# Kernel optimization log

Measured on AMD Instinct MI355X. Metric: run time of the kernel, lower is better.

The kernel has to match this reference:

```python
import jax, jax.numpy as jnp
import numpy as np

EPS = 1e-5  # PyTorch BatchNorm2d default eps


def _batchnorm(x, gamma, beta):
    # training-mode BN over (N, T, V) per channel; x: [N, C, T, V]
    mean = jnp.mean(x, axis=(0, 2, 3), keepdims=True)
    var = jnp.var(x, axis=(0, 2, 3), keepdims=True)
    inv = jax.lax.rsqrt(var + EPS)
    return (x - mean) * inv * gamma[None, :, None, None] + beta[None, :, None, None]


def setup_inputs() -> dict:
    key = jax.random.key(0)
    ks = jax.random.split(key, 8)
    N, Cin, Cout, T, V, S = 64, 64, 128, 300, 25, 3
    x = jax.random.normal(ks[0], (N, Cin, T, V), dtype=jnp.float32)
    A = jax.random.uniform(ks[1], (S, V, V), dtype=jnp.float32)
    # per-subset 1x1 conv weights/biases (kaiming-ish scale)
    W = jax.random.normal(ks[2], (S, Cout, Cin), dtype=jnp.float32) / np.sqrt(Cin)
    b = jax.random.normal(ks[3], (S, Cout), dtype=jnp.float32) * 0.01
    alpha = jnp.zeros((1,), dtype=jnp.float32)
    bn_gamma = jnp.ones((Cout,), dtype=jnp.float32)
    bn_beta = jnp.zeros((Cout,), dtype=jnp.float32)
    # residual down path (in_channels != out_channels): conv1x1 + BN
    down_W = jax.random.normal(ks[4], (Cout, Cin), dtype=jnp.float32) / np.sqrt(Cin)
    down_b = jax.random.normal(ks[5], (Cout,), dtype=jnp.float32) * 0.01
    down_gamma = jnp.ones((Cout,), dtype=jnp.float32)
    down_beta = jnp.zeros((Cout,), dtype=jnp.float32)
    return {
        "x": x, "A": A, "W": W, "b": b, "alpha": alpha,
        "bn_gamma": bn_gamma, "bn_beta": bn_beta,
        "down_W": down_W, "down_b": down_b,
        "down_gamma": down_gamma, "down_beta": down_beta,
    }


def reference(x, A, W, b, alpha, bn_gamma, bn_beta, down_W, down_b, down_gamma, down_beta):
    V = x.shape[-1]
    eye = jnp.eye(V, dtype=x.dtype)
    A_adj = A + alpha[0] * eye[None]  # [S, V, V]
    # sum_s conv1x1_s( x @ A_s ): fuse adjacency matmul, 1x1 conv, subset sum
    y_agg = jnp.einsum('nctv,svw,soc->notw', x, A_adj, W)
    y_agg = y_agg + jnp.sum(b, axis=0)[None, :, None, None]
    y = _batchnorm(y_agg, bn_gamma, bn_beta)
    # residual down: 1x1 conv + BN (in_channels != out_channels)
    res = jnp.einsum('nctv,oc->notv', x, down_W) + down_b[None, :, None, None]
    res = _batchnorm(res, down_gamma, down_beta)
    return jax.nn.relu(y + res)
```

## Files before the change

kernel.cpp:

```cpp
#include <hip/hip_runtime.h>
#include <hip/hip_bf16.h>

#define N_   64
#define CIN  64
#define COUT 128
#define T_   300
#define V_   25
#define S_   3
#define NTV  (N_ * T_ * V_)

#define TS     10
#define NTB    (T_ / TS)
#define NBLK   (N_ * NTB)
#define RED_ROWS   64
#define RED_BLOCKS (NBLK / RED_ROWS)

#define WS_P    0
#define WS_P2   (WS_P + NBLK * 512)
#define WS_COEF (WS_P2 + RED_BLOCKS * 512)
#define WS_WF   (WS_COEF + 512)
#define WS_WSF  (WS_WF + 16384)
#define WS_AF   (WS_WSF + 16384)

typedef __attribute__((ext_vector_type(8))) short short8;
typedef __attribute__((ext_vector_type(4))) float f32x4;

__device__ __forceinline__ unsigned short bfbits(float f) {
    union { __hip_bfloat16 h; unsigned short u; } cv;
    cv.h = __float2bfloat16(f);
    return cv.u;
}
__device__ __forceinline__ unsigned int pack2(float lo, float hi) {
    return (unsigned int)bfbits(lo) | ((unsigned int)bfbits(hi) << 16);
}

__device__ __forceinline__ int zoff(int nl, int k) {
    int slot = (k >> 3) ^ (nl & 31);
    return nl * 512 + slot * 16 + (k & 7) * 2;
}

__global__ __launch_bounds__(256) void k_prep(const float* __restrict__ W,
                                              const float* __restrict__ dW,
                                              const float* __restrict__ A,
                                              const float* __restrict__ alpha,
                                              unsigned short* __restrict__ Wf,
                                              unsigned short* __restrict__ Af) {
    int i = blockIdx.x * 256 + threadIdx.x;
    {
        int j = i & 7, lane = (i >> 3) & 63, ks = (i >> 9) & 7;
        int of = (i >> 12) & 1, oh = i >> 13;
        int o = oh * 32 + of * 16 + (lane & 15);
        int k = ks * 32 + (lane >> 4) * 8 + j;
        float wv = (k < 192) ? W[(k >> 6) * (COUT * CIN) + o * CIN + (k & 63)]
                             : dW[o * CIN + (k - 192)];
        Wf[i] = bfbits(wv);
    }
    if (i < 4096) {
        int j = i & 7, lane = (i >> 3) & 63, wf = (i >> 9) & 1, s = i >> 10;
        int v = (lane >> 4) * 8 + j, w = wf * 16 + (lane & 15);
        float av;
        if (s < 3)
            av = (v < V_ && w < V_)
                   ? A[(s * V_ + v) * V_ + w] + ((v == w) ? alpha[0] : 0.f)
                   : 0.f;
        else
            av = (v == w && v < V_) ? 1.f : 0.f;
        Af[i] = bfbits(av);
    }
}

__global__ __launch_bounds__(256) void k_prep2(const float* __restrict__ W,
                                               const float* __restrict__ dW,
                                               const float* __restrict__ coef,
                                               unsigned short* __restrict__ Wsf) {
    int i = blockIdx.x * 256 + threadIdx.x;
    int j = i & 7, lane = (i >> 3) & 63, ks = (i >> 9) & 7;
    int of = (i >> 12) & 1, oh = i >> 13;
    int o = oh * 32 + of * 16 + (lane & 15);
    int k = ks * 32 + (lane >> 4) * 8 + j;
    float wv = (k < 192) ? W[(k >> 6) * (COUT * CIN) + o * CIN + (k & 63)]
                         : dW[o * CIN + (k - 192)];
    float sc = (k < 192) ? coef[o] : coef[COUT + o];
    Wsf[i] = bfbits(wv * sc);
}

struct XRaw { f32x4 a0, a1; float s; };

__device__ __forceinline__ XRaw load_raw(const float* __restrict__ base, int lq) {
    XRaw r;
    if (lq < 3) {
        r.a0 = *(const f32x4*)(base + lq * 8);
        r.a1 = *(const f32x4*)(base + lq * 8 + 4);
        r.s = 0.f;
    } else {
        r.s = base[24];
        r.a0 = (f32x4){0.f, 0.f, 0.f, 0.f};
        r.a1 = (f32x4){0.f, 0.f, 0.f, 0.f};
    }
    return r;
}

__device__ __forceinline__ short8 cvt_xfr(const XRaw& x, int lq) {
    short8 r;
    if (lq < 3) {
#pragma unroll
        for (int j = 0; j < 4; ++j) {
            r[j]     = (short)bfbits(x.a0[j]);
            r[4 + j] = (short)bfbits(x.a1[j]);
        }
    } else {
        r[0] = (short)bfbits(x.s);
#pragma unroll
        for (int j = 1; j < 8; ++j) r[j] = 0;
    }
    return r;
}

__device__ __forceinline__ void stage(char* zb, const unsigned short* Alds,
                                      short8 xfr, int oh, int lq, int lr, int lane) {
    const f32x4 zero = {0.f, 0.f, 0.f, 0.f};
#pragma unroll
    for (int s = 0; s < 4; ++s)
#pragma unroll
        for (int wf = 0; wf < 2; ++wf) {
            short8 af = *(const short8*)(Alds + ((s * 2 + wf) * 64 + lane) * 8);
            f32x4 d = __builtin_amdgcn_mfma_f32_16x16x32_bf16(xfr, af, zero, 0, 0, 0);
            unsigned long long pk = (unsigned long long)pack2(d[0], d[1])
                                  | ((unsigned long long)pack2(d[2], d[3]) << 32);
            int row = wf * 16 + lr;
            int k = s * 64 + oh * 16 + lq * 4;
            *(unsigned long long*)(zb + zoff(row, k)) = pk;
        }
}

template<bool STATS, int MINW>
__global__ __launch_bounds__(256, MINW) void k_gemm(
    const float* __restrict__ x, const unsigned short* __restrict__ Wf,
    const unsigned short* __restrict__ Af, const float* __restrict__ coef,
    float* __restrict__ P, float* __restrict__ out)
{
    __shared__ __align__(16) unsigned short Zt[2][32 * 256];
    __shared__ __align__(16) unsigned short Alds[8 * 64 * 8];

    const int tid = threadIdx.x;
    const int oh = tid >> 6, lane = tid & 63;
    const int lq = lane >> 4, lr = lane & 15;

    const int bid = blockIdx.x;
    const int n = bid / NTB, tb = bid % NTB;
    const int t0 = tb * TS;

    for (int i = tid; i < 512; i += 256)
        *(short8*)(Alds + i * 8) = *(const short8*)(Af + i * 8);

    short8 wfr[2][8];
#pragma unroll
    for (int of = 0; of < 2; ++of)
#pragma unroll
        for (int ks = 0; ks < 8; ++ks)
            wfr[of][ks] = *(const short8*)(Wf + (((oh * 2 + of) * 8 + ks) * 64 + lane) * 8);

    float c0v[2] = {0.f, 0.f};
    if (!STATS) {
        c0v[0] = coef[2 * COUT + oh * 32 + lr];
        c0v[1] = coef[2 * COUT + oh * 32 + 16 + lr];
    }

    float sy[2] = {0.f, 0.f}, sy2[2] = {0.f, 0.f};
    float sr[2] = {0.f, 0.f}, sr2[2] = {0.f, 0.f};

    const int c = oh * 16 + lr;
    const float* xrow = x + ((size_t)(n * CIN + c) * T_) * V_;

    __syncthreads();

    {
        XRaw r0 = load_raw(xrow + (size_t)t0 * V_, lq);
        stage((char*)Zt[0], Alds, cvt_xfr(r0, lq), oh, lq, lr, lane);
    }
    XRaw slotA = load_raw(xrow + (size_t)(t0 + 1) * V_, lq);

    const f32x4 zero = {0.f, 0.f, 0.f, 0.f};

    for (int tt = 0; tt < TS; ++tt) {
        const int t = t0 + tt;
        char* zb = (char*)Zt[tt & 1];
        __syncthreads();

        XRaw slotB;
        if (tt + 2 < TS) slotB = load_raw(xrow + (size_t)(t + 2) * V_, lq);
        else { slotB.a0 = zero; slotB.a1 = zero; slotB.s = 0.f; }

        if (tt + 1 < TS)
            stage((char*)Zt[(tt + 1) & 1], Alds, cvt_xfr(slotA, lq), oh, lq, lr, lane);

        f32x4 acc[2][2];

        if constexpr (STATS) {
#pragma unroll
            for (int ks = 6; ks < 8; ++ks) {
                short8 za[2];
                za[0] = *(const short8*)(zb + zoff(lr, ks * 32 + lq * 8));
                za[1] = *(const short8*)(zb + zoff(16 + lr, ks * 32 + lq * 8));
#pragma unroll
                for (int mf = 0; mf < 2; ++mf)
#pragma unroll
                    for (int of = 0; of < 2; ++of)
                        acc[mf][of] = __builtin_amdgcn_mfma_f32_16x16x32_bf16(
                            za[mf], wfr[of][ks], ks == 6 ? zero : acc[mf][of], 0, 0, 0);
            }
#pragma unroll
            for (int of = 0; of < 2; ++of)
#pragma unroll
                for (int mf = 0; mf < 2; ++mf)
#pragma unroll
                    for (int r = 0; r < 4; ++r) {
                        float rv = acc[mf][of][r];
                        sr[of] += rv; sr2[of] = fmaf(rv, rv, sr2[of]);
                    }
#pragma unroll
            for (int ks = 0; ks < 6; ++ks) {
                short8 za[2];
                za[0] = *(const short8*)(zb + zoff(lr, ks * 32 + lq * 8));
                za[1] = *(const short8*)(zb + zoff(16 + lr, ks * 32 + lq * 8));
#pragma unroll
                for (int mf = 0; mf < 2; ++mf)
#pragma unroll
                    for (int of = 0; of < 2; ++of)
                        acc[mf][of] = __builtin_amdgcn_mfma_f32_16x16x32_bf16(
                            za[mf], wfr[of][ks], ks == 0 ? zero : acc[mf][of], 0, 0, 0);
            }
#pragma unroll
            for (int of = 0; of < 2; ++of)
#pragma unroll
                for (int mf = 0; mf < 2; ++mf)
#pragma unroll
                    for (int r = 0; r < 4; ++r) {
                        float yv = acc[mf][of][r];
                        sy[of] += yv; sy2[of] = fmaf(yv, yv, sy2[of]);
                    }
        } else {
#pragma unroll
            for (int ks = 0; ks < 8; ++ks) {
                short8 za[2];
                za[0] = *(const short8*)(zb + zoff(lr, ks * 32 + lq * 8));
                za[1] = *(const short8*)(zb + zoff(16 + lr, ks * 32 + lq * 8));
#pragma unroll
                for (int mf = 0; mf < 2; ++mf)
#pragma unroll
                    for (int of = 0; of < 2; ++of)
                        acc[mf][of] = __builtin_amdgcn_mfma_f32_16x16x32_bf16(
                            za[mf], wfr[of][ks], ks == 0 ? zero : acc[mf][of], 0, 0, 0);
            }
#pragma unroll
            for (int of = 0; of < 2; ++of) {
                int o = oh * 32 + of * 16 + lr;
                float* rowp = out + ((size_t)(n * COUT + o) * T_ + t) * V_;
                f32x4 v0;
#pragma unroll
                for (int r = 0; r < 4; ++r) v0[r] = fmaxf(acc[0][of][r] + c0v[of], 0.f);
                *(f32x4*)(rowp + lq * 4) = v0;
                if (lq < 2) {
                    f32x4 v1;
#pragma unroll
                    for (int r = 0; r < 4; ++r) v1[r] = fmaxf(acc[1][of][r] + c0v[of], 0.f);
                    *(f32x4*)(rowp + 16 + lq * 4) = v1;
                } else if (lq == 2) {
                    rowp[24] = fmaxf(acc[1][of][0] + c0v[of], 0.f);
                }
            }
        }

        slotA.a0 = slotB.a0; slotA.a1 = slotB.a1; slotA.s = slotB.s;
    }

    if constexpr (STATS) {
#pragma unroll
        for (int of = 0; of < 2; ++of) {
            sy[of]  += __shfl_xor(sy[of], 16);  sy[of]  += __shfl_xor(sy[of], 32);
            sy2[of] += __shfl_xor(sy2[of], 16); sy2[of] += __shfl_xor(sy2[of], 32);
            sr[of]  += __shfl_xor(sr[of], 16);  sr[of]  += __shfl_xor(sr[of], 32);
            sr2[of] += __shfl_xor(sr2[of], 16); sr2[of] += __shfl_xor(sr2[of], 32);
        }
        if (lq == 0) {
            float* p = P + (size_t)bid * 512;
#pragma unroll
            for (int of = 0; of < 2; ++of) {
                int o = oh * 32 + of * 16 + lr;
                p[o] = sy[of]; p[128 + o] = sy2[of];
                p[256 + o] = sr[of]; p[384 + o] = sr2[of];
            }
        }
    }
}

__global__ __launch_bounds__(256) void k_red(const float* __restrict__ P,
                                             float* __restrict__ P2) {
    const int tid = threadIdx.x;
    float a0 = 0.f, a1 = 0.f;
    const int row0 = blockIdx.x * RED_ROWS;
    for (int r = 0; r < RED_ROWS; ++r) {
        const float* p = P + (size_t)(row0 + r) * 512;
        a0 += p[tid];
        a1 += p[256 + tid];
    }
    P2[blockIdx.x * 512 + tid] = a0;
    P2[blockIdx.x * 512 + 256 + tid] = a1;
}

__global__ __launch_bounds__(128) void k_coef(
    const float* __restrict__ P2, const float* __restrict__ gamma,
    const float* __restrict__ beta, const float* __restrict__ dgamma,
    const float* __restrict__ dbeta, const float* __restrict__ b,
    const float* __restrict__ db, float* __restrict__ coef) {
    const int o = threadIdx.x;
    float sy = 0.f, sy2 = 0.f, sr = 0.f, sr2 = 0.f;
    for (int r2 = 0; r2 < RED_BLOCKS; ++r2) {
        const float* p = P2 + r2 * 512;
        sy += p[o]; sy2 += p[128 + o]; sr += p[256 + o]; sr2 += p[384 + o];
    }
    const float bsum = b[o] + b[COUT + o] + b[2 * COUT + o];
    const float dbo = db[o];
    float syb  = sy + (float)NTV * bsum;
    float sy2b = sy2 + 2.f * bsum * sy + (float)NTV * bsum * bsum;
    float srb  = sr + (float)NTV * dbo;
    float sr2b = sr2 + 2.f * dbo * sr + (float)NTV * dbo * dbo;
    const float invn = 1.f / (float)NTV;
    float my = syb * invn, mr = srb * invn;
    float vy = fmaf(-my, my, sy2b * invn);
    float vr = fmaf(-mr, mr, sr2b * invn);
    float ay = rsqrtf(vy + 1e-5f) * gamma[o];
    float ar = rsqrtf(vr + 1e-5f) * dgamma[o];
    float c0 = beta[o] - my * ay + dbeta[o] - mr * ar + ay * bsum + ar * dbo;
    coef[o] = ay; coef[COUT + o] = ar; coef[2 * COUT + o] = c0;
}

extern "C" void kernel_launch(void* const* d_in, const int* in_sizes, int n_in,
                              void* d_out, int out_size, void* d_ws, size_t ws_size,
                              hipStream_t stream) {
    const float* x      = (const float*)d_in[0];
    const float* A      = (const float*)d_in[1];
    const float* W      = (const float*)d_in[2];
    const float* b      = (const float*)d_in[3];
    const float* alpha  = (const float*)d_in[4];
    const float* gamma  = (const float*)d_in[5];
    const float* beta   = (const float*)d_in[6];
    const float* dW     = (const float*)d_in[7];
    const float* db     = (const float*)d_in[8];
    const float* dgamma = (const float*)d_in[9];
    const float* dbeta  = (const float*)d_in[10];

    float* ws   = (float*)d_ws;
    float* P    = ws + WS_P;
    float* P2   = ws + WS_P2;
    float* coef = ws + WS_COEF;
    unsigned short* Wf  = (unsigned short*)(ws + WS_WF);
    unsigned short* Wsf = (unsigned short*)(ws + WS_WSF);
    unsigned short* Af  = (unsigned short*)(ws + WS_AF);
    float* out  = (float*)d_out;

    k_prep<<<128, 256, 0, stream>>>(W, dW, A, alpha, Wf, Af);
    k_gemm<true, 3><<<NBLK, 256, 0, stream>>>(x, Wf, Af, nullptr, P, nullptr);
    k_red<<<RED_BLOCKS, 256, 0, stream>>>(P, P2);
    k_coef<<<1, 128, 0, stream>>>(P2, gamma, beta, dgamma, dbeta, b, db, coef);
    k_prep2<<<128, 256, 0, stream>>>(W, dW, coef, Wsf);
    k_gemm<false, 4><<<NBLK, 256, 0, stream>>>(x, Wsf, Af, coef, nullptr, out);
}
```

Before: 258.4 us.

## Use packed bf16 conversion, lighter LDS barriers, block swizzle, uniform launch bounds

Converts pairs of floats to bf16 with the packed two-wide intrinsic instead of element by element. Replaces __syncthreads with an explicit lgkmcnt wait plus s_barrier, so outstanding global loads are not drained at each step. Remaps block ids in an interleaved pattern to change the order in which blocks touch memory, and sets the second gemm pass to a minimum of 3 waves instead of 4. These are several small tweaks aimed at conversion cost, barrier stalls and register pressure; the lower occupancy hint could help or hurt the output pass.

Measured after the change: 221.9 us, median of 2. -14.1%, faster.

```diff
diff --git a/kernel.cpp b/kernel.cpp
--- a/kernel.cpp
+++ b/kernel.cpp
@@ -25,13 +25,17 @@
 typedef __attribute__((ext_vector_type(8))) short short8;
 typedef __attribute__((ext_vector_type(4))) float f32x4;
 
+#define LDS_BARRIER() asm volatile("s_waitcnt lgkmcnt(0)\n\ts_barrier" ::: "memory")
+
 __device__ __forceinline__ unsigned short bfbits(float f) {
     union { __hip_bfloat16 h; unsigned short u; } cv;
     cv.h = __float2bfloat16(f);
     return cv.u;
 }
 __device__ __forceinline__ unsigned int pack2(float lo, float hi) {
-    return (unsigned int)bfbits(lo) | ((unsigned int)bfbits(hi) << 16);
+    union { __hip_bfloat162 h2; unsigned int u; } cv;
+    cv.h2 = __float22bfloat162_rn(float2{lo, hi});
+    return cv.u;
 }
 
 __device__ __forceinline__ int zoff(int nl, int k) {
@@ -101,19 +105,17 @@
 }
 
 __device__ __forceinline__ short8 cvt_xfr(const XRaw& x, int lq) {
-    short8 r;
+    union { short8 s8; unsigned int u[4]; } b;
     if (lq < 3) {
-#pragma unroll
-        for (int j = 0; j < 4; ++j) {
-            r[j]     = (short)bfbits(x.a0[j]);
-            r[4 + j] = (short)bfbits(x.a1[j]);
-        }
+        b.u[0] = pack2(x.a0[0], x.a0[1]);
+        b.u[1] = pack2(x.a0[2], x.a0[3]);
+        b.u[2] = pack2(x.a1[0], x.a1[1]);
+        b.u[3] = pack2(x.a1[2], x.a1[3]);
     } else {
-        r[0] = (short)bfbits(x.s);
-#pragma unroll
-        for (int j = 1; j < 8; ++j) r[j] = 0;
-    }
-    return r;
+        b.u[0] = pack2(x.s, 0.f);
+        b.u[1] = 0; b.u[2] = 0; b.u[3] = 0;
+    }
+    return b.s8;
 }
 
 __device__ __forceinline__ void stage(char* zb, const unsigned short* Alds,
@@ -133,8 +135,8 @@
         }
 }
 
-template<bool STATS, int MINW>
-__global__ __launch_bounds__(256, MINW) void k_gemm(
+template<bool STATS>
+__global__ __launch_bounds__(256, 3) void k_gemm(
     const float* __restrict__ x, const unsigned short* __restrict__ Wf,
     const unsigned short* __restrict__ Af, const float* __restrict__ coef,
     float* __restrict__ P, float* __restrict__ out)
@@ -146,7 +148,8 @@
     const int oh = tid >> 6, lane = tid & 63;
     const int lq = lane >> 4, lr = lane & 15;
 
-    const int bid = blockIdx.x;
+    const int bid0 = blockIdx.x;
+    const int bid = (bid0 & 7) * (NBLK / 8) + (bid0 >> 3);
     const int n = bid / NTB, tb = bid % NTB;
     const int t0 = tb * TS;
 
@@ -172,7 +175,7 @@
     const int c = oh * 16 + lr;
     const float* xrow = x + ((size_t)(n * CIN + c) * T_) * V_;
 
-    __syncthreads();
+    LDS_BARRIER();
 
     {
         XRaw r0 = load_raw(xrow + (size_t)t0 * V_, lq);
@@ -185,7 +188,7 @@
     for (int tt = 0; tt < TS; ++tt) {
         const int t = t0 + tt;
         char* zb = (char*)Zt[tt & 1];
-        __syncthreads();
+        LDS_BARRIER();
 
         XRaw slotB;
         if (tt + 2 < TS) slotB = load_raw(xrow + (size_t)(t + 2) * V_, lq);
@@ -360,9 +363,9 @@
     float* out  = (float*)d_out;
 
     k_prep<<<128, 256, 0, stream>>>(W, dW, A, alpha, Wf, Af);
-    k_gemm<true, 3><<<NBLK, 256, 0, stream>>>(x, Wf, Af, nullptr, P, nullptr);
+    k_gemm<true><<<NBLK, 256, 0, stream>>>(x, Wf, Af, nullptr, P, nullptr);
     k_red<<<RED_BLOCKS, 256, 0, stream>>>(P, P2);
     k_coef<<<1, 128, 0, stream>>>(P2, gamma, beta, dgamma, dbeta, b, db, coef);
     k_prep2<<<128, 256, 0, stream>>>(W, dW, coef, Wsf);
-    k_gemm<false, 4><<<NBLK, 256, 0, stream>>>(x, Wsf, Af, coef, nullptr, out);
-}
+    k_gemm<false><<<NBLK, 256, 0, stream>>>(x, Wsf, Af, coef, nullptr, out);
+}
```
